# Performance work log

Measured on AMD Instinct MI355X. Metric: run time of the kernel, lower is better.

## Reference

```python
import jax, jax.numpy as jnp
import numpy as np
from jax import lax

B, C, H, W = 16, 64, 64, 64
K = 3                  # kernel_size
D_IN = C * K           # moe input dim = 192
D_OUT = 128            # out_channels
N_EXP = 8
TOP_K = 2
N_SHARED = 1


def setup_inputs() -> dict:
    key = jax.random.key(0)
    ks = jax.random.split(key, 7)
    x = jax.random.normal(ks[0], (B, C, H, W), dtype=jnp.float32)
    # depthwise conv: groups=C, each input channel -> K output channels
    conv_w = jax.random.normal(ks[1], (D_IN, 1, K, K), dtype=jnp.float32) * 0.1
    router_w = jax.random.normal(ks[2], (D_IN, N_EXP), dtype=jnp.float32) * 0.05
    w_experts = jax.random.normal(ks[3], (N_EXP, D_IN, D_OUT), dtype=jnp.float32) * 0.05
    b_experts = jnp.zeros((N_EXP, D_OUT), dtype=jnp.float32)
    w_shared = jax.random.normal(ks[4], (N_SHARED, D_IN, D_OUT), dtype=jnp.float32) * 0.05
    b_shared = jnp.zeros((N_SHARED, D_OUT), dtype=jnp.float32)
    return {"x": x, "conv_w": conv_w, "router_w": router_w,
            "w_experts": w_experts, "b_experts": b_experts,
            "w_shared": w_shared, "b_shared": b_shared}


def _moe_conv2d(x, conv_w, router_w, w_experts, b_experts, w_shared, b_shared):
    pad = K // 2
    # depthwise conv (B,C,H,W) -> (B, C*K, H, W)
    x_conv = lax.conv_general_dilated(
        x, conv_w, window_strides=(1, 1), padding=[(pad, pad), (pad, pad)],
        feature_group_count=C, dimension_numbers=("NCHW", "OIHW", "NCHW"))
    # flatten to token stream (B*H*W, D_IN)
    tokens = x_conv.transpose(0, 2, 3, 1).reshape(-1, D_IN)
    # router: softmax probs, top-k gating renormalized over selected experts
    logits = tokens @ router_w                       # (T, E)
    probs = jax.nn.softmax(logits, axis=-1)
    top_v, top_i = lax.top_k(probs, TOP_K)           # (T, k)
    gates = top_v / jnp.sum(top_v, axis=-1, keepdims=True)
    # all-expert outputs then gather the selected k per token
    expert_out = jnp.einsum("ti,eio->teo", tokens, w_experts) + b_experts  # (T, E, O)
    sel = jnp.take_along_axis(expert_out, top_i[:, :, None], axis=1)       # (T, k, O)
    y_flat = jnp.einsum("tk,tko->to", gates, sel)
    # shared experts applied to every token
    shared = jnp.einsum("ti,sio->tso", tokens, w_shared) + b_shared        # (T, S, O)
    y_flat = y_flat + jnp.sum(shared, axis=1)
    # back to feature map (B, O, H, W)
    return y_flat.reshape(B, H, W, D_OUT).transpose(0, 3, 1, 2)


def reference(x, conv_w, router_w, w_experts, b_experts, w_shared, b_shared):
    return _moe_conv2d(x, conv_w, router_w, w_experts, b_experts, w_shared, b_shared)
```

## Files before the change

kernel.cpp:

```cpp
#include <hip/hip_runtime.h>
#include <math.h>

#define BB   16
#define CC   64
#define DIN  192
#define DOUT 128
#define NEXP 8
#define NMAT 9
#define NTOK 65536
#define CAP  65568
#define SLABROWS 65552

#define TOKSTRIDE 200
#define HALFSTRIDE 104
#define LOGSTRIDE 9
#define CSTRIDE 136

typedef short bf16x8 __attribute__((ext_vector_type(8)));
typedef float f32x4  __attribute__((ext_vector_type(4)));

#define WS_TOK   0u
#define WS_WT    25165824u
#define WS_CNT   25608192u
#define WS_RT    25608256u
#define WS_RG    27706432u
#define WS_SLAB  29804608u
#define WS_TOTAL 63367232u
#define LPHALF 524288

__device__ __forceinline__ unsigned short f2bf(float f) {
    union { float f; unsigned u; } v; v.f = f;
    unsigned u = v.u;
    u += 0x7fffu + ((u >> 16) & 1u);
    return (unsigned short)(u >> 16);
}
__device__ __forceinline__ float bf2f(unsigned short s) {
    union { unsigned u; float f; } v; v.u = ((unsigned)s) << 16;
    return v.f;
}

__global__ __launch_bounds__(256)
void k1a_conv(const float* __restrict__ x,
              const float* __restrict__ conv_w,
              const float* __restrict__ router_w,
              unsigned short* __restrict__ tokbuf,
              float* __restrict__ lpart,
              int* __restrict__ cnt)
{
    __shared__ __attribute__((aligned(16))) unsigned short tokbf[64 * HALFSTRIDE];
    __shared__ float logits[64 * LOGSTRIDE];
    __shared__ __attribute__((aligned(16))) float xs[2][16 * 192];

    const int tid   = threadIdx.x;
    const int bid   = blockIdx.x;
    const int bh    = bid >> 1;
    const int chalf = bid & 1;
    const int b     = bh >> 6;
    const int h     = bh & 63;

    if (bid == 0 && tid < 16) cnt[tid] = 0;
    for (int idx = tid; idx < 64 * LOGSTRIDE; idx += 256) logits[idx] = 0.f;

    const int   h0  = (h > 0)  ? (h - 1) : 0;
    const int   h2  = (h < 63) ? (h + 1) : 63;
    const float mh0 = (h > 0)  ? 1.f : 0.f;
    const float mh2 = (h < 63) ? 1.f : 0.f;

    const int sc[3]  = { (0*256+tid)/48, (1*256+tid)/48, (2*256+tid)/48 };
    int srow[3], sseg[3];
    #pragma unroll
    for (int q = 0; q < 3; ++q) {
        int rem = (q * 256 + tid) % 48;
        srow[q] = rem >> 4; sseg[q] = rem & 15;
    }
    const float* xb = x + (size_t)b * CC * 4096;

    {
        float4 st[3];
        #pragma unroll
        for (int q = 0; q < 3; ++q) {
            int hh = (srow[q] == 0) ? h0 : ((srow[q] == 1) ? h : h2);
            st[q] = *(const float4*)(xb + ((size_t)(chalf * 32 + sc[q]) * 64 + hh) * 64
                                        + sseg[q] * 4);
        }
        #pragma unroll
        for (int q = 0; q < 3; ++q)
            *(float4*)&xs[0][sc[q] * 192 + srow[q] * 64 + sseg[q] * 4] = st[q];
    }
    __syncthreads();

    const int w  = tid & 63;
    const int cq = __builtin_amdgcn_readfirstlane(tid >> 6);

    const int   wm  = (w == 0)  ? 0  : (w - 1);
    const int   wp  = (w == 63) ? 63 : (w + 1);
    const float mwm = (w == 0)  ? 0.f : 1.f;
    const float mwp = (w == 63) ? 0.f : 1.f;

    float lacc[8];
    #pragma unroll
    for (int e = 0; e < 8; ++e) lacc[e] = 0.f;

    float4 st1[3];
    #pragma unroll
    for (int q = 0; q < 3; ++q) {
        int hh = (srow[q] == 0) ? h0 : ((srow[q] == 1) ? h : h2);
        st1[q] = *(const float4*)(xb + ((size_t)(chalf * 32 + 16 + sc[q]) * 64 + hh) * 64
                                     + sseg[q] * 4);
    }

    #pragma unroll
    for (int ch = 0; ch < 2; ++ch) {
        const float* xsc = xs[ch];
        #pragma unroll
        for (int i = 0; i < 4; ++i) {
            int cc = cq * 4 + i;
            int cl = ch * 16 + cc;
            const float* r0 = xsc + cc * 192;
            const float* r1 = r0 + 64;
            const float* r2 = r0 + 128;
            float x00 = r0[wm], x01 = r0[w], x02 = r0[wp];
            float x10 = r1[wm], x11 = r1[w], x12 = r1[wp];
            float x20 = r2[wm], x21 = r2[w], x22 = r2[wp];
            x00 *= mh0 * mwm; x01 *= mh0; x02 *= mh0 * mwp;
            x10 *= mwm;                    x12 *= mwp;
            x20 *= mh2 * mwm; x21 *= mh2; x22 *= mh2 * mwp;

            #pragma unroll
            for (int j = 0; j < 3; ++j) {
                int fl = 3 * cl + j;
                int f  = chalf * 96 + fl;
                const float* w9 = conv_w + f * 9;
                float acc = x00 * w9[0] + x01 * w9[1] + x02 * w9[2]
                          + x10 * w9[3] + x11 * w9[4] + x12 * w9[5]
                          + x20 * w9[6] + x21 * w9[7] + x22 * w9[8];
                tokbf[w * HALFSTRIDE + fl] = f2bf(acc);
                const float* rwf = router_w + f * 8;
                #pragma unroll
                for (int e = 0; e < 8; ++e) lacc[e] += acc * rwf[e];
            }
        }
        if (ch == 0) {
            #pragma unroll
            for (int q = 0; q < 3; ++q)
                *(float4*)&xs[1][sc[q] * 192 + srow[q] * 64 + sseg[q] * 4] = st1[q];
            __syncthreads();
        }
    }

    #pragma unroll
    for (int e = 0; e < 8; ++e)
        atomicAdd(&logits[w * LOGSTRIDE + e], lacc[e]);
    __syncthreads();

    for (int idx = tid; idx < 512; idx += 256) {
        int wtok = idx >> 3, e = idx & 7;
        lpart[(size_t)chalf * LPHALF + ((size_t)bh * 64 + wtok) * 8 + e] =
            logits[wtok * LOGSTRIDE + e];
    }
    for (int idx = tid; idx < 768; idx += 256) {
        int row = idx / 12, seg = idx - row * 12;
        *(bf16x8*)(tokbuf + (size_t)(bh * 64 + row) * 192 + chalf * 96 + seg * 8) =
            *(const bf16x8*)(tokbf + row * HALFSTRIDE + seg * 8);
    }
}

__global__ __launch_bounds__(256)
void k1b_route(const float* __restrict__ lpart,
               int* __restrict__ cnt,
               int* __restrict__ rowtok, float* __restrict__ rowgate,
               const float* __restrict__ w_experts,
               const float* __restrict__ w_shared,
               unsigned short* __restrict__ wt)
{
    __shared__ int lcnt[8];
    __shared__ int lbase[8];

    const int tid = threadIdx.x;
    const int blk = blockIdx.x;
    const int t   = blk * 256 + tid;

    if (tid < 8) lcnt[tid] = 0;
    __syncthreads();

    const float* p0 = lpart + (size_t)t * 8;
    const float* p1 = lpart + LPHALF + (size_t)t * 8;
    float l[8];
    #pragma unroll
    for (int e = 0; e < 8; ++e) l[e] = p0[e] + p1[e];

    int e0 = 0; float l0 = l[0];
    #pragma unroll
    for (int e = 1; e < 8; ++e) if (l[e] > l0) { l0 = l[e]; e0 = e; }
    int e1 = -1; float l1 = -INFINITY;
    #pragma unroll
    for (int e = 0; e < 8; ++e) {
        if (e == e0) continue;
        if (l[e] > l1) { l1 = l[e]; e1 = e; }
    }
    float g0 = 1.f / (1.f + expf(l1 - l0));
    float g1 = 1.f - g0;

    int r0 = atomicAdd(&lcnt[e0], 1);
    int r1 = atomicAdd(&lcnt[e1], 1);
    __syncthreads();
    if (tid < 8) lbase[tid] = atomicAdd(&cnt[tid], lcnt[tid]);
    __syncthreads();

    int p0i = e0 * CAP + lbase[e0] + r0;
    int p1i = e1 * CAP + lbase[e1] + r1;
    rowtok[p0i]  = t;
    rowgate[p0i] = g0;
    rowtok[p1i]  = t | (1 << 20);
    rowgate[p1i] = g1;

    {
        int base = blk * 864;
        for (int q = 0; q < 4; ++q) {
            int idx = base + q * 256 + tid;
            if (idx < 221184 && (q * 256 + tid) < 864) {
                int e = idx / 24576, rem = idx - e * 24576;
                int n = rem / DIN,  k  = rem - n * DIN;
                const float* src = (e < 8) ? (w_experts + (size_t)e * DIN * DOUT)
                                           : w_shared;
                wt[idx] = f2bf(src[k * DOUT + n]);
            }
        }
    }
}

__global__ __launch_bounds__(256)
void k4_routed(const unsigned short* __restrict__ tokbuf,
               const unsigned short* __restrict__ wt,
               const float* __restrict__ b_experts,
               const int* __restrict__ cnt,
               const int* __restrict__ rowtok, const float* __restrict__ rowgate,
               unsigned short* __restrict__ slab)
{
    __shared__ __attribute__((aligned(16))) unsigned short atile[2][16 * TOKSTRIDE];
    __shared__ __attribute__((aligned(16))) unsigned short ctile[2][16 * CSTRIDE];
    __shared__ int   stok[2][16];
    __shared__ float sgate[2][16];

    const int tid  = threadIdx.x;
    const int e    = blockIdx.x >> 8;
    const int jb   = blockIdx.x & 255;
    const int wave = tid >> 6;
    const int lane = tid & 63;
    const int m16  = lane & 15, quad = lane >> 4;
    const int o0   = (wave * 2 + 0) * 16 + m16;
    const int o1   = (wave * 2 + 1) * 16 + m16;

    const unsigned short* wb = wt + (size_t)e * DOUT * DIN;
    bf16x8 bfr0[6], bfr1[6];
    #pragma unroll
    for (int ks = 0; ks < 6; ++ks) {
        bfr0[ks] = *(const bf16x8*)(wb + (size_t)o0 * DIN + ks * 32 + quad * 8);
        bfr1[ks] = *(const bf16x8*)(wb + (size_t)o1 * DIN + ks * 32 + quad * 8);
    }
    const float be0 = b_experts[e * DOUT + o0];
    const float be1 = b_experts[e * DOUT + o1];

    const int cnt_e  = cnt[e];
    const int ntiles = (cnt_e + 15) >> 4;
    const int*   rt = rowtok  + e * CAP;
    const float* rg = rowgate + e * CAP;

    const int r0i = tid / 24,        s0i = tid - r0i * 24;
    const int r1i = (tid + 256) / 24, s1i = (tid + 256) - r1i * 24;
    const bool has1 = (tid + 256) < 384;

    if (jb < ntiles) {
        int base = jb * 16;
        if (tid < 16) {
            int r = base + tid;
            bool ok = (r < cnt_e);
            stok[0][tid]  = ok ? rt[r] : NTOK;
            sgate[0][tid] = ok ? rg[r] : 0.f;
        }
        {
            int ra = base + r0i;
            int raw = (ra < cnt_e) ? rt[ra] : NTOK;
            *(bf16x8*)&atile[0][r0i * TOKSTRIDE + s0i * 8] =
                *(const bf16x8*)(tokbuf + (size_t)(raw & 0x1FFFF) * 192 + s0i * 8);
            if (has1) {
                int rb = base + r1i;
                int rawb = (rb < cnt_e) ? rt[rb] : NTOK;
                *(bf16x8*)&atile[0][r1i * TOKSTRIDE + s1i * 8] =
                    *(const bf16x8*)(tokbuf + (size_t)(rawb & 0x1FFFF) * 192 + s1i * 8);
            }
        }
    }
    __syncthreads();

    int buf = 0;
    for (int j = jb; j < ntiles; j += 256, buf ^= 1) {
        const int jn = j + 256;
        const bool more = (jn < ntiles);

        bf16x8 nx0 = {0,0,0,0,0,0,0,0}, nx1 = {0,0,0,0,0,0,0,0};
        int nmt = NTOK; float nmg = 0.f;
        if (more) {
            int base = jn * 16;
            if (tid < 16) {
                int r = base + tid;
                bool ok = (r < cnt_e);
                nmt = ok ? rt[r] : NTOK;
                nmg = ok ? rg[r] : 0.f;
            }
            int ra = base + r0i;
            int rawa = (ra < cnt_e) ? rt[ra] : NTOK;
            nx0 = *(const bf16x8*)(tokbuf + (size_t)(rawa & 0x1FFFF) * 192 + s0i * 8);
            if (has1) {
                int rb = base + r1i;
                int rawb = (rb < cnt_e) ? rt[rb] : NTOK;
                nx1 = *(const bf16x8*)(tokbuf + (size_t)(rawb & 0x1FFFF) * 192 + s1i * 8);
            }
        }

        bf16x8 a[6];
        #pragma unroll
        for (int ks = 0; ks < 6; ++ks)
            a[ks] = *(const bf16x8*)&atile[buf][m16 * TOKSTRIDE + ks * 32 + quad * 8];

        f32x4 acc0 = {0.f, 0.f, 0.f, 0.f};
        f32x4 acc1 = {0.f, 0.f, 0.f, 0.f};
        #pragma unroll
        for (int ks = 0; ks < 6; ++ks) {
            acc0 = __builtin_amdgcn_mfma_f32_16x16x32_bf16(a[ks], bfr0[ks], acc0, 0, 0, 0);
            acc1 = __builtin_amdgcn_mfma_f32_16x16x32_bf16(a[ks], bfr1[ks], acc1, 0, 0, 0);
        }

        #pragma unroll
        for (int i = 0; i < 4; ++i) {
            int   row = quad * 4 + i;
            float g   = sgate[buf][row];
            ctile[buf][row * CSTRIDE + o0] = f2bf(g * (acc0[i] + be0));
            ctile[buf][row * CSTRIDE + o1] = f2bf(g * (acc1[i] + be1));
        }

        if (more) {
            if (tid < 16) { stok[buf ^ 1][tid] = nmt; sgate[buf ^ 1][tid] = nmg; }
            *(bf16x8*)&atile[buf ^ 1][r0i * TOKSTRIDE + s0i * 8] = nx0;
            if (has1) *(bf16x8*)&atile[buf ^ 1][r1i * TOKSTRIDE + s1i * 8] = nx1;
        }
        __syncthreads();

        {
            int row = tid >> 4, chk = tid & 15;
            int raw = stok[buf][row];
            int t    = raw & 0x1FFFF;
            int slot = raw >> 20;
            *(bf16x8*)(slab + (size_t)slot * SLABROWS * DOUT
                            + (size_t)t * DOUT + chk * 8) =
                *(const bf16x8*)&ctile[buf][row * CSTRIDE + chk * 8];
        }
    }
}

__global__ __launch_bounds__(256)
void k3_shared(const unsigned short* __restrict__ tokbuf,
               const unsigned short* __restrict__ wt,
               const unsigned short* __restrict__ slab,
               const float* __restrict__ b_shared,
               float* __restrict__ out)
{
    __shared__ float out_lds[32 * 129];

    const int tid  = threadIdx.x;
    const int bid  = blockIdx.x;
    const int bh   = bid >> 1;
    const int wh   = bid & 1;
    const int b    = bh >> 6;
    const int h    = bh & 63;
    const int wave = tid >> 6, lane = tid & 63;
    const int mt   = wave >> 1, nh = wave & 1;
    const int m16  = lane & 15, quad = lane >> 4;
    const int t0   = bh * 64 + wh * 32;

    bf16x8 pv0[2], pv1[2];
    {
        const unsigned short* s0 = slab;
        const unsigned short* s1 = slab + (size_t)SLABROWS * DOUT;
        #pragma unroll
        for (int it = 0; it < 2; ++it) {
            int idx = it * 256 + tid;
            int tl = idx >> 4, chk = idx & 15;
            size_t gt = (size_t)t0 + tl;
            pv0[it] = *(const bf16x8*)(s0 + gt * DOUT + chk * 8);
            pv1[it] = *(const bf16x8*)(s1 + gt * DOUT + chk * 8);
        }
    }

    const unsigned short* ap =
        tokbuf + (size_t)(t0 + mt * 16 + m16) * 192 + quad * 8;
    bf16x8 a[6];
    #pragma unroll
    for (int ks = 0; ks < 6; ++ks) a[ks] = *(const bf16x8*)(ap + ks * 32);

    const unsigned short* wsh = wt + (size_t)8 * DOUT * DIN;

    bf16x8 bcur[6], bnxt[6];
    {
        int o = (nh * 4 + 0) * 16 + m16;
        const unsigned short* bp = wsh + (size_t)o * DIN + quad * 8;
        #pragma unroll
        for (int ks = 0; ks < 6; ++ks) bcur[ks] = *(const bf16x8*)(bp + ks * 32);
    }
    #pragma unroll
    for (int nb2 = 0; nb2 < 4; ++nb2) {
        if (nb2 < 3) {
            int on = (nh * 4 + nb2 + 1) * 16 + m16;
            const unsigned short* bp = wsh + (size_t)on * DIN + quad * 8;
            #pragma unroll
            for (int ks = 0; ks < 6; ++ks) bnxt[ks] = *(const bf16x8*)(bp + ks * 32);
        }
        int o = (nh * 4 + nb2) * 16 + m16;
        f32x4 acc = {0.f, 0.f, 0.f, 0.f};
        #pragma unroll
        for (int ks = 0; ks < 6; ++ks)
            acc = __builtin_amdgcn_mfma_f32_16x16x32_bf16(a[ks], bcur[ks], acc, 0, 0, 0);
        float bs = b_shared[o];
        #pragma unroll
        for (int i = 0; i < 4; ++i) {
            int tloc = mt * 16 + quad * 4 + i;
            out_lds[tloc * 129 + o] = acc[i] + bs;
        }
        #pragma unroll
        for (int ks = 0; ks < 6; ++ks) bcur[ks] = bnxt[ks];
    }
    __syncthreads();

    #pragma unroll
    for (int it = 0; it < 2; ++it) {
        int idx = it * 256 + tid;
        int tl = idx >> 4, chk = idx & 15;
        float* dst = &out_lds[tl * 129 + chk * 8];
        #pragma unroll
        for (int q = 0; q < 8; ++q)
            dst[q] += bf2f((unsigned short)pv0[it][q])
                    + bf2f((unsigned short)pv1[it][q]);
    }
    __syncthreads();

    float* outp = out + ((size_t)b * DOUT) * 4096 + h * 64 + wh * 32;
    for (int idx = tid; idx < 32 * DOUT; idx += 256) {
        int wloc = idx & 31, o = idx >> 5;
        outp[(size_t)o * 4096 + wloc] = out_lds[wloc * 129 + o];
    }
}

#define OUTSTRIDE 129
#define MAXROWS 320
#define MAXTILES 20

__global__ __launch_bounds__(256)
void moe_conv2d_mfma(const float* __restrict__ x,
                     const float* __restrict__ conv_w,
                     const float* __restrict__ router_w,
                     const unsigned short* __restrict__ wt,
                     const float* __restrict__ b_experts,
                     const float* __restrict__ b_shared,
                     float* __restrict__ out)
{
    __shared__ __attribute__((aligned(16))) unsigned short tokbf[64 * TOKSTRIDE];
    __shared__ float out_lds[64 * OUTSTRIDE];
    __shared__ float rw[DIN * NEXP];
    __shared__ float logits[64 * LOGSTRIDE];
    __shared__ float sg0[64], sg1[64];
    __shared__ int   se0[64], se1[64];
    __shared__ int   rowtok[MAXROWS];
    __shared__ float rowgate[MAXROWS];
    __shared__ int   cbuf[NMAT];
    __shared__ int   tilexp[MAXTILES], tilebase[MAXTILES];
    __shared__ int   ntiles_s;

    const int tid = threadIdx.x;
    const int bh  = blockIdx.x;
    const int b   = bh >> 6;
    const int h   = bh & 63;

    for (int idx = tid; idx < DIN * NEXP; idx += 256) rw[idx] = router_w[idx];
    for (int idx = tid; idx < 64 * LOGSTRIDE; idx += 256) logits[idx] = 0.f;
    __syncthreads();
    {
        const int w  = tid & 63;
        const int fq = tid >> 6;
        float lacc[8];
        #pragma unroll
        for (int e = 0; e < 8; ++e) lacc[e] = 0.f;
        for (int i = 0; i < 48; ++i) {
            int f = i * 4 + fq;
            int c = f / 3;
            const float* wp    = conv_w + f * 9;
            const float* xbase = x + ((size_t)(b * 64 + c) * 64) * 64;
            float acc = 0.f;
            #pragma unroll
            for (int kh = 0; kh < 3; ++kh) {
                int hh = h + kh - 1;
                if (hh < 0 || hh > 63) continue;
                const float* xrow = xbase + hh * 64;
                #pragma unroll
                for (int kw = 0; kw < 3; ++kw) {
                    int ww = w + kw - 1;
                    if (ww < 0 || ww > 63) continue;
                    acc += xrow[ww] * wp[kh * 3 + kw];
                }
            }
            tokbf[w * TOKSTRIDE + f] = f2bf(acc);
            const float* rwf = rw + f * 8;
            #pragma unroll
            for (int e = 0; e < 8; ++e) lacc[e] += acc * rwf[e];
        }
        #pragma unroll
        for (int e = 0; e < 8; ++e)
            atomicAdd(&logits[w * LOGSTRIDE + e], lacc[e]);
    }
    __syncthreads();
    if (tid < 64) {
        int w = tid;
        float l[8];
        #pragma unroll
        for (int e = 0; e < 8; ++e) l[e] = logits[w * LOGSTRIDE + e];
        int e0 = 0; float l0 = l[0];
        #pragma unroll
        for (int e = 1; e < 8; ++e) if (l[e] > l0) { l0 = l[e]; e0 = e; }
        int e1 = -1; float l1 = -INFINITY;
        #pragma unroll
        for (int e = 0; e < 8; ++e) {
            if (e == e0) continue;
            if (l[e] > l1) { l1 = l[e]; e1 = e; }
        }
        float g0 = 1.f / (1.f + expf(l1 - l0));
        sg0[w] = g0; sg1[w] = 1.f - g0;
        se0[w] = e0; se1[w] = e1;
    }
    __syncthreads();
    for (int idx = tid; idx < 64 * DOUT; idx += 256) {
        int t = idx >> 7, o = idx & 127;
        out_lds[t * OUTSTRIDE + o] = b_shared[o]
            + sg0[t] * b_experts[se0[t] * DOUT + o]
            + sg1[t] * b_experts[se1[t] * DOUT + o];
    }
    if (tid < 8) {
        int c = 0;
        for (int t = 0; t < 64; ++t) c += (se0[t] == tid) + (se1[t] == tid);
        cbuf[tid] = c;
    } else if (tid == 8) cbuf[8] = 64;
    __syncthreads();
    if (tid < NMAT) {
        int e = tid;
        int start = 0, tb = 0;
        for (int e2 = 0; e2 < e; ++e2) {
            int ce = cbuf[e2];
            int tl = (ce + 15) >> 4;
            start += tl << 4; tb += tl;
        }
        int ce = cbuf[e];
        int tl = (ce + 15) >> 4;
        for (int j = 0; j < tl; ++j) { tilexp[tb + j] = e; tilebase[tb + j] = start + (j << 4); }
        if (e == 8) ntiles_s = tb + tl;
        int j = 0;
        if (e < 8) {
            for (int t = 0; t < 64; ++t) {
                if (se0[t] == e) { rowtok[start + j] = t; rowgate[start + j] = sg0[t]; ++j; }
                if (se1[t] == e) { rowtok[start + j] = t; rowgate[start + j] = sg1[t]; ++j; }
            }
        } else {
            for (int t = 0; t < 64; ++t) { rowtok[start + j] = t; rowgate[start + j] = 1.f; ++j; }
        }
        for (; j < (tl << 4); ++j) { rowtok[start + j] = 0; rowgate[start + j] = 0.f; }
    }
    __syncthreads();
    {
        const int wave = tid >> 6;
        const int lane = tid & 63;
        const int m16  = lane & 15;
        const int quad = lane >> 4;
        const int nt   = ntiles_s;
        for (int ti = wave; ti < nt; ti += 4) {
            int e    = tilexp[ti];
            int base = tilebase[ti];
            int tA = rowtok[base + m16];
            bf16x8 a[6];
            #pragma unroll
            for (int ks = 0; ks < 6; ++ks)
                a[ks] = *(const bf16x8*)(tokbf + tA * TOKSTRIDE + ks * 32 + quad * 8);
            int st[4]; float sgt[4];
            #pragma unroll
            for (int i2 = 0; i2 < 4; ++i2) {
                int r = base + quad * 4 + i2;
                st[i2] = rowtok[r]; sgt[i2] = rowgate[r];
            }
            const unsigned short* we = wt + (size_t)e * DOUT * DIN;
            for (int n = 0; n < 8; ++n) {
                const unsigned short* wp = we + (size_t)(n * 16 + m16) * DIN + quad * 8;
                f32x4 acc = {0.f, 0.f, 0.f, 0.f};
                #pragma unroll
                for (int ks = 0; ks < 6; ++ks) {
                    bf16x8 bfr2 = *(const bf16x8*)(wp + ks * 32);
                    acc = __builtin_amdgcn_mfma_f32_16x16x32_bf16(a[ks], bfr2, acc, 0, 0, 0);
                }
                int ncol = n * 16 + m16;
                #pragma unroll
                for (int i2 = 0; i2 < 4; ++i2)
                    atomicAdd(&out_lds[st[i2] * OUTSTRIDE + ncol], sgt[i2] * acc[i2]);
            }
        }
    }
    __syncthreads();
    {
        float* outp = out + (((size_t)b * DOUT) * 64 + h) * 64;
        for (int idx = tid; idx < 64 * DOUT; idx += 256) {
            int w = idx & 63, o = idx >> 6;
            outp[(size_t)o * 4096 + w] = out_lds[w * OUTSTRIDE + o];
        }
    }
}

__global__ __launch_bounds__(256)
void prep_weights_only(const float* __restrict__ w_experts,
                       const float* __restrict__ w_shared,
                       unsigned short* __restrict__ wt)
{
    int e = blockIdx.x;
    const float* src = (e < 8) ? (w_experts + (size_t)e * DIN * DOUT) : w_shared;
    unsigned short* dst = wt + (size_t)e * DOUT * DIN;
    for (int idx = threadIdx.x; idx < DOUT * DIN; idx += 256) {
        int n = idx / DIN, k = idx - n * DIN;
        dst[idx] = f2bf(src[k * DOUT + n]);
    }
}

extern "C" void kernel_launch(void* const* d_in, const int* in_sizes, int n_in,
                              void* d_out, int out_size, void* d_ws, size_t ws_size,
                              hipStream_t stream)
{
    const float* x         = (const float*)d_in[0];
    const float* conv_w    = (const float*)d_in[1];
    const float* router_w  = (const float*)d_in[2];
    const float* w_experts = (const float*)d_in[3];
    const float* b_experts = (const float*)d_in[4];
    const float* w_shared  = (const float*)d_in[5];
    const float* b_shared  = (const float*)d_in[6];
    float* out = (float*)d_out;
    char* ws = (char*)d_ws;

    if (ws_size >= WS_TOTAL) {
        unsigned short* tokbuf  = (unsigned short*)(ws + WS_TOK);
        unsigned short* wt      = (unsigned short*)(ws + WS_WT);
        int*            cnt     = (int*)(ws + WS_CNT);
        int*            rowtok  = (int*)(ws + WS_RT);
        float*          rowgate = (float*)(ws + WS_RG);
        unsigned short* slab    = (unsigned short*)(ws + WS_SLAB);
        float*          lpart   = (float*)(ws + WS_SLAB);

        k1a_conv<<<dim3(2048), dim3(256), 0, stream>>>(
            x, conv_w, router_w, tokbuf, lpart, cnt);
        k1b_route<<<dim3(256), dim3(256), 0, stream>>>(
            lpart, cnt, rowtok, rowgate, w_experts, w_shared, wt);
        k4_routed<<<dim3(2048), dim3(256), 0, stream>>>(
            tokbuf, wt, b_experts, cnt, rowtok, rowgate, slab);
        k3_shared<<<dim3(2048), dim3(256), 0, stream>>>(
            tokbuf, wt, slab, b_shared, out);
    } else {
        unsigned short* wt = (unsigned short*)ws;
        prep_weights_only<<<dim3(NMAT), dim3(256), 0, stream>>>(w_experts, w_shared, wt);
        moe_conv2d_mfma<<<dim3(1024), dim3(256), 0, stream>>>(
            x, conv_w, router_w, wt, b_experts, b_shared, out);
    }
}
```

Measured before the change: 179.3 us.

## Fuse conv with routing and fold shared expert into routed GEMM kernel

The conv and routing kernels are merged, so each block computes its 32 tokens' full 192-dim features and logits, does top-2 selection and expert-slot assignment in place, and no longer writes and re-reads partial logits. The counter reset moves to a memset. When the workspace is large enough, the shared expert runs as a ninth dense 'expert' inside the routed MFMA kernel, writing to a third slab. A light combine kernel then sums the three slabs and transposes to NCHW. This trades the heavier shared-GEMM epilogue for extra slab traffic, and it needs a larger workspace or else falls back to the old path.

```diff
diff --git a/kernel.cpp b/kernel.cpp
--- a/kernel.cpp
+++ b/kernel.cpp
@@ -12,7 +12,6 @@
 #define SLABROWS 65552
 
 #define TOKSTRIDE 200
-#define HALFSTRIDE 104
 #define LOGSTRIDE 9
 #define CSTRIDE 136
 
@@ -25,8 +24,8 @@
 #define WS_RT    25608256u
 #define WS_RG    27706432u
 #define WS_SLAB  29804608u
-#define WS_TOTAL 63367232u
-#define LPHALF 524288
+#define WS_TOTAL  63367232u
+#define WS_TOTAL3 80148544u
 
 __device__ __forceinline__ unsigned short f2bf(float f) {
     union { float f; unsigned u; } v; v.f = f;
@@ -40,202 +39,173 @@
 }
 
 __global__ __launch_bounds__(256)
-void k1a_conv(const float* __restrict__ x,
-              const float* __restrict__ conv_w,
-              const float* __restrict__ router_w,
-              unsigned short* __restrict__ tokbuf,
-              float* __restrict__ lpart,
-              int* __restrict__ cnt)
-{
-    __shared__ __attribute__((aligned(16))) unsigned short tokbf[64 * HALFSTRIDE];
-    __shared__ float logits[64 * LOGSTRIDE];
-    __shared__ __attribute__((aligned(16))) float xs[2][16 * 192];
-
-    const int tid   = threadIdx.x;
-    const int bid   = blockIdx.x;
-    const int bh    = bid >> 1;
-    const int chalf = bid & 1;
-    const int b     = bh >> 6;
-    const int h     = bh & 63;
-
-    if (bid == 0 && tid < 16) cnt[tid] = 0;
-    for (int idx = tid; idx < 64 * LOGSTRIDE; idx += 256) logits[idx] = 0.f;
-
-    const int   h0  = (h > 0)  ? (h - 1) : 0;
-    const int   h2  = (h < 63) ? (h + 1) : 63;
-    const float mh0 = (h > 0)  ? 1.f : 0.f;
-    const float mh2 = (h < 63) ? 1.f : 0.f;
-
-    const int sc[3]  = { (0*256+tid)/48, (1*256+tid)/48, (2*256+tid)/48 };
-    int srow[3], sseg[3];
-    #pragma unroll
-    for (int q = 0; q < 3; ++q) {
-        int rem = (q * 256 + tid) % 48;
-        srow[q] = rem >> 4; sseg[q] = rem & 15;
-    }
-    const float* xb = x + (size_t)b * CC * 4096;
-
-    {
-        float4 st[3];
-        #pragma unroll
-        for (int q = 0; q < 3; ++q) {
-            int hh = (srow[q] == 0) ? h0 : ((srow[q] == 1) ? h : h2);
-            st[q] = *(const float4*)(xb + ((size_t)(chalf * 32 + sc[q]) * 64 + hh) * 64
-                                        + sseg[q] * 4);
-        }
-        #pragma unroll
-        for (int q = 0; q < 3; ++q)
-            *(float4*)&xs[0][sc[q] * 192 + srow[q] * 64 + sseg[q] * 4] = st[q];
-    }
-    __syncthreads();
-
-    const int w  = tid & 63;
-    const int cq = __builtin_amdgcn_readfirstlane(tid >> 6);
-
-    const int   wm  = (w == 0)  ? 0  : (w - 1);
-    const int   wp  = (w == 63) ? 63 : (w + 1);
-    const float mwm = (w == 0)  ? 0.f : 1.f;
-    const float mwp = (w == 63) ? 0.f : 1.f;
-
-    float lacc[8];
-    #pragma unroll
-    for (int e = 0; e < 8; ++e) lacc[e] = 0.f;
-
-    float4 st1[3];
-    #pragma unroll
-    for (int q = 0; q < 3; ++q) {
-        int hh = (srow[q] == 0) ? h0 : ((srow[q] == 1) ? h : h2);
-        st1[q] = *(const float4*)(xb + ((size_t)(chalf * 32 + 16 + sc[q]) * 64 + hh) * 64
-                                     + sseg[q] * 4);
-    }
-
-    #pragma unroll
-    for (int ch = 0; ch < 2; ++ch) {
-        const float* xsc = xs[ch];
-        #pragma unroll
-        for (int i = 0; i < 4; ++i) {
-            int cc = cq * 4 + i;
-            int cl = ch * 16 + cc;
-            const float* r0 = xsc + cc * 192;
-            const float* r1 = r0 + 64;
-            const float* r2 = r0 + 128;
-            float x00 = r0[wm], x01 = r0[w], x02 = r0[wp];
-            float x10 = r1[wm], x11 = r1[w], x12 = r1[wp];
-            float x20 = r2[wm], x21 = r2[w], x22 = r2[wp];
-            x00 *= mh0 * mwm; x01 *= mh0; x02 *= mh0 * mwp;
-            x10 *= mwm;                    x12 *= mwp;
-            x20 *= mh2 * mwm; x21 *= mh2; x22 *= mh2 * mwp;
-
-            #pragma unroll
-            for (int j = 0; j < 3; ++j) {
-                int fl = 3 * cl + j;
-                int f  = chalf * 96 + fl;
-                const float* w9 = conv_w + f * 9;
-                float acc = x00 * w9[0] + x01 * w9[1] + x02 * w9[2]
-                          + x10 * w9[3] + x11 * w9[4] + x12 * w9[5]
-                          + x20 * w9[6] + x21 * w9[7] + x22 * w9[8];
-                tokbf[w * HALFSTRIDE + fl] = f2bf(acc);
-                const float* rwf = router_w + f * 8;
-                #pragma unroll
-                for (int e = 0; e < 8; ++e) lacc[e] += acc * rwf[e];
-            }
-        }
-        if (ch == 0) {
-            #pragma unroll
-            for (int q = 0; q < 3; ++q)
-                *(float4*)&xs[1][sc[q] * 192 + srow[q] * 64 + sseg[q] * 4] = st1[q];
-            __syncthreads();
-        }
-    }
-
-    #pragma unroll
-    for (int e = 0; e < 8; ++e)
-        atomicAdd(&logits[w * LOGSTRIDE + e], lacc[e]);
-    __syncthreads();
-
-    for (int idx = tid; idx < 512; idx += 256) {
-        int wtok = idx >> 3, e = idx & 7;
-        lpart[(size_t)chalf * LPHALF + ((size_t)bh * 64 + wtok) * 8 + e] =
-            logits[wtok * LOGSTRIDE + e];
-    }
-    for (int idx = tid; idx < 768; idx += 256) {
-        int row = idx / 12, seg = idx - row * 12;
-        *(bf16x8*)(tokbuf + (size_t)(bh * 64 + row) * 192 + chalf * 96 + seg * 8) =
-            *(const bf16x8*)(tokbf + row * HALFSTRIDE + seg * 8);
-    }
-}
-
-__global__ __launch_bounds__(256)
-void k1b_route(const float* __restrict__ lpart,
+void k1a_fused(const float* __restrict__ x,
+               const float* __restrict__ conv_w,
+               const float* __restrict__ router_w,
+               unsigned short* __restrict__ tokbuf,
                int* __restrict__ cnt,
                int* __restrict__ rowtok, float* __restrict__ rowgate,
                const float* __restrict__ w_experts,
                const float* __restrict__ w_shared,
                unsigned short* __restrict__ wt)
 {
-    __shared__ int lcnt[8];
-    __shared__ int lbase[8];
-
-    const int tid = threadIdx.x;
-    const int blk = blockIdx.x;
-    const int t   = blk * 256 + tid;
+    __shared__ __attribute__((aligned(16))) float xs[2][1920];
+    __shared__ __attribute__((aligned(16))) unsigned short tokbf[32 * TOKSTRIDE];
+    __shared__ float logits[32 * LOGSTRIDE];
+    __shared__ int lcnt[8], lbase[8];
+
+    const int tid   = threadIdx.x;
+    const int bid   = blockIdx.x;
+    const int bh    = bid >> 1;
+    const int wh    = bid & 1;
+    const int b     = bh >> 6;
+    const int h     = bh & 63;
+    const int wbase = wh * 32;
+    const int t0    = bh * 64 + wbase;
 
     if (tid < 8) lcnt[tid] = 0;
-    __syncthreads();
-
-    const float* p0 = lpart + (size_t)t * 8;
-    const float* p1 = lpart + LPHALF + (size_t)t * 8;
-    float l[8];
-    #pragma unroll
-    for (int e = 0; e < 8; ++e) l[e] = p0[e] + p1[e];
-
-    int e0 = 0; float l0 = l[0];
-    #pragma unroll
-    for (int e = 1; e < 8; ++e) if (l[e] > l0) { l0 = l[e]; e0 = e; }
-    int e1 = -1; float l1 = -INFINITY;
-    #pragma unroll
-    for (int e = 0; e < 8; ++e) {
-        if (e == e0) continue;
-        if (l[e] > l1) { l1 = l[e]; e1 = e; }
-    }
-    float g0 = 1.f / (1.f + expf(l1 - l0));
-    float g1 = 1.f - g0;
-
-    int r0 = atomicAdd(&lcnt[e0], 1);
-    int r1 = atomicAdd(&lcnt[e1], 1);
+    for (int idx = tid; idx < 32 * LOGSTRIDE; idx += 256) logits[idx] = 0.f;
+
+    const int   h0  = (h > 0)  ? (h - 1) : 0;
+    const int   h2  = (h < 63) ? (h + 1) : 63;
+    const float mh0 = (h > 0)  ? 1.f : 0.f;
+    const float mh2 = (h < 63) ? 1.f : 0.f;
+
+    const float* xb = x + (size_t)b * CC * 4096;
+
+    int sc[2], sr[2], ss[2], sc4[2]; bool sv[2];
+    #pragma unroll
+    for (int q = 0; q < 2; ++q) {
+        int idx = q * 256 + tid;
+        sv[q] = idx < 480;
+        int c16 = idx / 30, rem = idx % 30;
+        sc[q] = c16; sr[q] = rem / 10; ss[q] = rem % 10;
+        int c4 = (wbase >> 2) + ss[q] - 1;
+        sc4[q] = c4 < 0 ? 0 : (c4 > 15 ? 15 : c4);
+    }
+
+    #pragma unroll
+    for (int q = 0; q < 2; ++q) if (sv[q]) {
+        int hh = (sr[q] == 0) ? h0 : ((sr[q] == 1) ? h : h2);
+        float4 v = *(const float4*)(xb + ((size_t)sc[q] * 64 + hh) * 64 + sc4[q] * 4);
+        *(float4*)&xs[0][sc[q] * 120 + sr[q] * 40 + ss[q] * 4] = v;
+    }
+    __syncthreads();
+
+    const int wloc = tid & 31;
+    const int cg   = tid >> 5;
+    const int w    = wbase + wloc;
+    const float mwm = (w == 0)  ? 0.f : 1.f;
+    const float mwp = (w == 63) ? 0.f : 1.f;
+
+    float lacc[8];
+    #pragma unroll
+    for (int e = 0; e < 8; ++e) lacc[e] = 0.f;
+
+    int buf = 0;
+    for (int ck = 0; ck < 4; ++ck) {
+        float4 st[2];
+        if (ck < 3) {
+            #pragma unroll
+            for (int q = 0; q < 2; ++q) if (sv[q]) {
+                int hh = (sr[q] == 0) ? h0 : ((sr[q] == 1) ? h : h2);
+                st[q] = *(const float4*)(xb + ((size_t)((ck + 1) * 16 + sc[q]) * 64 + hh) * 64
+                                            + sc4[q] * 4);
+            }
+        }
+        #pragma unroll
+        for (int i = 0; i < 2; ++i) {
+            int cc = cg * 2 + i;
+            int c  = ck * 16 + cc;
+            const float* r0 = &xs[buf][cc * 120];
+            const float* r1 = r0 + 40;
+            const float* r2 = r0 + 80;
+            float x00 = r0[wloc+3], x01 = r0[wloc+4], x02 = r0[wloc+5];
+            float x10 = r1[wloc+3], x11 = r1[wloc+4], x12 = r1[wloc+5];
+            float x20 = r2[wloc+3], x21 = r2[wloc+4], x22 = r2[wloc+5];
+            x00 *= mh0 * mwm; x01 *= mh0; x02 *= mh0 * mwp;
+            x10 *= mwm;                    x12 *= mwp;
+            x20 *= mh2 * mwm; x21 *= mh2; x22 *= mh2 * mwp;
+            #pragma unroll
+            for (int j = 0; j < 3; ++j) {
+                int f = 3 * c + j;
+                const float* w9 = conv_w + f * 9;
+                float acc = x00 * w9[0] + x01 * w9[1] + x02 * w9[2]
+                          + x10 * w9[3] + x11 * w9[4] + x12 * w9[5]
+                          + x20 * w9[6] + x21 * w9[7] + x22 * w9[8];
+                tokbf[wloc * TOKSTRIDE + f] = f2bf(acc);
+                const float* rwf = router_w + f * 8;
+                #pragma unroll
+                for (int e = 0; e < 8; ++e) lacc[e] += acc * rwf[e];
+            }
+        }
+        if (ck < 3) {
+            #pragma unroll
+            for (int q = 0; q < 2; ++q) if (sv[q])
+                *(float4*)&xs[buf ^ 1][sc[q] * 120 + sr[q] * 40 + ss[q] * 4] = st[q];
+            __syncthreads();
+            buf ^= 1;
+        }
+    }
+    #pragma unroll
+    for (int e = 0; e < 8; ++e)
+        atomicAdd(&logits[wloc * LOGSTRIDE + e], lacc[e]);
+    __syncthreads();
+
+    int e0r = 0, e1r = 0, r0r = 0, r1r = 0; float g0r = 0.f, g1r = 0.f;
+    if (tid < 32) {
+        float l[8];
+        #pragma unroll
+        for (int e = 0; e < 8; ++e) l[e] = logits[tid * LOGSTRIDE + e];
+        int e0 = 0; float l0 = l[0];
+        #pragma unroll
+        for (int e = 1; e < 8; ++e) if (l[e] > l0) { l0 = l[e]; e0 = e; }
+        int e1 = -1; float l1 = -INFINITY;
+        #pragma unroll
+        for (int e = 0; e < 8; ++e) {
+            if (e == e0) continue;
+            if (l[e] > l1) { l1 = l[e]; e1 = e; }
+        }
+        float g0 = 1.f / (1.f + expf(l1 - l0));
+        e0r = e0; e1r = e1; g0r = g0; g1r = 1.f - g0;
+        r0r = atomicAdd(&lcnt[e0], 1);
+        r1r = atomicAdd(&lcnt[e1], 1);
+    }
     __syncthreads();
     if (tid < 8) lbase[tid] = atomicAdd(&cnt[tid], lcnt[tid]);
     __syncthreads();
-
-    int p0i = e0 * CAP + lbase[e0] + r0;
-    int p1i = e1 * CAP + lbase[e1] + r1;
-    rowtok[p0i]  = t;
-    rowgate[p0i] = g0;
-    rowtok[p1i]  = t | (1 << 20);
-    rowgate[p1i] = g1;
-
-    {
-        int base = blk * 864;
-        for (int q = 0; q < 4; ++q) {
-            int idx = base + q * 256 + tid;
-            if (idx < 221184 && (q * 256 + tid) < 864) {
-                int e = idx / 24576, rem = idx - e * 24576;
-                int n = rem / DIN,  k  = rem - n * DIN;
-                const float* src = (e < 8) ? (w_experts + (size_t)e * DIN * DOUT)
-                                           : w_shared;
-                wt[idx] = f2bf(src[k * DOUT + n]);
-            }
-        }
+    if (tid < 32) {
+        int t = t0 + tid;
+        int i0 = e0r * CAP + lbase[e0r] + r0r;
+        rowtok[i0] = t;              rowgate[i0] = g0r;
+        int i1 = e1r * CAP + lbase[e1r] + r1r;
+        rowtok[i1] = t | (1 << 20);  rowgate[i1] = g1r;
+    }
+
+    #pragma unroll
+    for (int q = 0; q < 3; ++q) {
+        int idx = q * 256 + tid;
+        int row = idx / 24, seg = idx - row * 24;
+        *(bf16x8*)(tokbuf + (size_t)(t0 + row) * 192 + seg * 8) =
+            *(const bf16x8*)(tokbf + row * TOKSTRIDE + seg * 8);
+    }
+    if (tid < 108) {
+        int idx = bid * 108 + tid;
+        int e = idx / 24576, rem = idx - e * 24576;
+        int n = rem / DIN, k = rem - n * DIN;
+        const float* src = (e < 8) ? (w_experts + (size_t)e * DIN * DOUT) : w_shared;
+        wt[idx] = f2bf(src[k * DOUT + n]);
     }
 }
 
 __global__ __launch_bounds__(256)
-void k4_routed(const unsigned short* __restrict__ tokbuf,
-               const unsigned short* __restrict__ wt,
-               const float* __restrict__ b_experts,
-               const int* __restrict__ cnt,
-               const int* __restrict__ rowtok, const float* __restrict__ rowgate,
-               unsigned short* __restrict__ slab)
+void k4_all(const unsigned short* __restrict__ tokbuf,
+            const unsigned short* __restrict__ wt,
+            const float* __restrict__ b_experts,
+            const float* __restrict__ b_shared,
+            const int* __restrict__ cnt,
+            const int* __restrict__ rowtok, const float* __restrict__ rowgate,
+            unsigned short* __restrict__ slab)
 {
     __shared__ __attribute__((aligned(16))) unsigned short atile[2][16 * TOKSTRIDE];
     __shared__ __attribute__((aligned(16))) unsigned short ctile[2][16 * CSTRIDE];
@@ -243,8 +213,11 @@
     __shared__ float sgate[2][16];
 
     const int tid  = threadIdx.x;
-    const int e    = blockIdx.x >> 8;
-    const int jb   = blockIdx.x & 255;
+    int e, jb, jstep;
+    if (blockIdx.x < 2048) { e = blockIdx.x >> 8; jb = blockIdx.x & 255; jstep = 256; }
+    else                   { e = 8; jb = blockIdx.x - 2048; jstep = 1024; }
+    const bool dense = (e == 8);
+
     const int wave = tid >> 6;
     const int lane = tid & 63;
     const int m16  = lane & 15, quad = lane >> 4;
@@ -258,34 +231,33 @@
         bfr0[ks] = *(const bf16x8*)(wb + (size_t)o0 * DIN + ks * 32 + quad * 8);
         bfr1[ks] = *(const bf16x8*)(wb + (size_t)o1 * DIN + ks * 32 + quad * 8);
     }
-    const float be0 = b_experts[e * DOUT + o0];
-    const float be1 = b_experts[e * DOUT + o1];
-
-    const int cnt_e  = cnt[e];
+    const float be0 = dense ? b_shared[o0] : b_experts[e * DOUT + o0];
+    const float be1 = dense ? b_shared[o1] : b_experts[e * DOUT + o1];
+
+    const int cnt_e  = dense ? NTOK : cnt[e];
     const int ntiles = (cnt_e + 15) >> 4;
     const int*   rt = rowtok  + e * CAP;
     const float* rg = rowgate + e * CAP;
 
-    const int r0i = tid / 24,        s0i = tid - r0i * 24;
+    const int r0i = tid / 24,         s0i = tid - r0i * 24;
     const int r1i = (tid + 256) / 24, s1i = (tid + 256) - r1i * 24;
     const bool has1 = (tid + 256) < 384;
+
+    #define FETCH_RAW(r) (dense ? ((r) | (2 << 20)) : (((r) < cnt_e) ? rt[r] : NTOK))
+    #define FETCH_G(r)   (dense ? 1.f : (((r) < cnt_e) ? rg[r] : 0.f))
 
     if (jb < ntiles) {
         int base = jb * 16;
         if (tid < 16) {
-            int r = base + tid;
-            bool ok = (r < cnt_e);
-            stok[0][tid]  = ok ? rt[r] : NTOK;
-            sgate[0][tid] = ok ? rg[r] : 0.f;
+            stok[0][tid]  = FETCH_RAW(base + tid);
+            sgate[0][tid] = FETCH_G(base + tid);
         }
         {
-            int ra = base + r0i;
-            int raw = (ra < cnt_e) ? rt[ra] : NTOK;
+            int rawa = FETCH_RAW(base + r0i);
             *(bf16x8*)&atile[0][r0i * TOKSTRIDE + s0i * 8] =
-                *(const bf16x8*)(tokbuf + (size_t)(raw & 0x1FFFF) * 192 + s0i * 8);
+                *(const bf16x8*)(tokbuf + (size_t)(rawa & 0x1FFFF) * 192 + s0i * 8);
             if (has1) {
-                int rb = base + r1i;
-                int rawb = (rb < cnt_e) ? rt[rb] : NTOK;
+                int rawb = FETCH_RAW(base + r1i);
                 *(bf16x8*)&atile[0][r1i * TOKSTRIDE + s1i * 8] =
                     *(const bf16x8*)(tokbuf + (size_t)(rawb & 0x1FFFF) * 192 + s1i * 8);
             }
@@ -294,26 +266,19 @@
     __syncthreads();
 
     int buf = 0;
-    for (int j = jb; j < ntiles; j += 256, buf ^= 1) {
-        const int jn = j + 256;
+    for (int j = jb; j < ntiles; j += jstep, buf ^= 1) {
+        const int jn = j + jstep;
         const bool more = (jn < ntiles);
 
         bf16x8 nx0 = {0,0,0,0,0,0,0,0}, nx1 = {0,0,0,0,0,0,0,0};
         int nmt = NTOK; float nmg = 0.f;
         if (more) {
             int base = jn * 16;
-            if (tid < 16) {
-                int r = base + tid;
-                bool ok = (r < cnt_e);
-                nmt = ok ? rt[r] : NTOK;
-                nmg = ok ? rg[r] : 0.f;
-            }
-            int ra = base + r0i;
-            int rawa = (ra < cnt_e) ? rt[ra] : NTOK;
+            if (tid < 16) { nmt = FETCH_RAW(base + tid); nmg = FETCH_G(base + tid); }
+            int rawa = FETCH_RAW(base + r0i);
             nx0 = *(const bf16x8*)(tokbuf + (size_t)(rawa & 0x1FFFF) * 192 + s0i * 8);
             if (has1) {
-                int rb = base + r1i;
-                int rawb = (rb < cnt_e) ? rt[rb] : NTOK;
+                int rawb = FETCH_RAW(base + r1i);
                 nx1 = *(const bf16x8*)(tokbuf + (size_t)(rawb & 0x1FFFF) * 192 + s1i * 8);
             }
         }
@@ -355,6 +320,49 @@
                             + (size_t)t * DOUT + chk * 8) =
                 *(const bf16x8*)&ctile[buf][row * CSTRIDE + chk * 8];
         }
+    }
+    #undef FETCH_RAW
+    #undef FETCH_G
+}
+
+__global__ __launch_bounds__(256)
+void k3_combine(const unsigned short* __restrict__ slab,
+                float* __restrict__ out)
+{
+    __shared__ float out_lds[32 * 129];
+
+    const int tid = threadIdx.x;
+    const int bid = blockIdx.x;
+    const int bh  = bid >> 1;
+    const int wh  = bid & 1;
+    const int b   = bh >> 6;
+    const int h   = bh & 63;
+    const int t0  = bh * 64 + wh * 32;
+
+    const unsigned short* s0 = slab;
+    const unsigned short* s1 = slab + (size_t)SLABROWS * DOUT;
+    const unsigned short* s2 = slab + (size_t)2 * SLABROWS * DOUT;
+
+    #pragma unroll
+    for (int it = 0; it < 2; ++it) {
+        int idx = it * 256 + tid;
+        int tl = idx >> 4, chk = idx & 15;
+        size_t gt = (size_t)t0 + tl;
+        bf16x8 v0 = *(const bf16x8*)(s0 + gt * DOUT + chk * 8);
+        bf16x8 v1 = *(const bf16x8*)(s1 + gt * DOUT + chk * 8);
+        bf16x8 v2 = *(const bf16x8*)(s2 + gt * DOUT + chk * 8);
+        float* dst = &out_lds[tl * 129 + chk * 8];
+        #pragma unroll
+        for (int q = 0; q < 8; ++q)
+            dst[q] = bf2f((unsigned short)v0[q]) + bf2f((unsigned short)v1[q])
+                   + bf2f((unsigned short)v2[q]);
+    }
+    __syncthreads();
+
+    float* outp = out + ((size_t)b * DOUT) * 4096 + h * 64 + wh * 32;
+    for (int idx = tid; idx < 32 * DOUT; idx += 256) {
+        int wloc = idx & 31, o = idx >> 5;
+        outp[(size_t)o * 4096 + wloc] = out_lds[wloc * 129 + o];
     }
 }
 
@@ -653,16 +661,21 @@
         int*            rowtok  = (int*)(ws + WS_RT);
         float*          rowgate = (float*)(ws + WS_RG);
         unsigned short* slab    = (unsigned short*)(ws + WS_SLAB);
-        float*          lpart   = (float*)(ws + WS_SLAB);
-
-        k1a_conv<<<dim3(2048), dim3(256), 0, stream>>>(
-            x, conv_w, router_w, tokbuf, lpart, cnt);
-        k1b_route<<<dim3(256), dim3(256), 0, stream>>>(
-            lpart, cnt, rowtok, rowgate, w_experts, w_shared, wt);
-        k4_routed<<<dim3(2048), dim3(256), 0, stream>>>(
-            tokbuf, wt, b_experts, cnt, rowtok, rowgate, slab);
-        k3_shared<<<dim3(2048), dim3(256), 0, stream>>>(
-            tokbuf, wt, slab, b_shared, out);
+
+        hipMemsetAsync(cnt, 0, 64, stream);
+        k1a_fused<<<dim3(2048), dim3(256), 0, stream>>>(
+            x, conv_w, router_w, tokbuf, cnt, rowtok, rowgate,
+            w_experts, w_shared, wt);
+        if (ws_size >= WS_TOTAL3) {
+            k4_all<<<dim3(3072), dim3(256), 0, stream>>>(
+                tokbuf, wt, b_experts, b_shared, cnt, rowtok, rowgate, slab);
+            k3_combine<<<dim3(2048), dim3(256), 0, stream>>>(slab, out);
+        } else {
+            k4_all<<<dim3(2048), dim3(256), 0, stream>>>(
+                tokbuf, wt, b_experts, b_shared, cnt, rowtok, rowgate, slab);
+            k3_shared<<<dim3(2048), dim3(256), 0, stream>>>(
+                tokbuf, wt, slab, b_shared, out);
+        }
     } else {
         unsigned short* wt = (unsigned short*)ws;
         prep_weights_only<<<dim3(NMAT), dim3(256), 0, stream>>>(w_experts, w_shared, wt);
```

Result: slower. 199.6 us (+11.3%).

## Fold shared-expert GEMM into routed kernel, add lightweight combine kernel

Applied to the files above, without the earlier changes.

The shared-expert matmul moves into the routed MFMA kernel as 1024 extra dense blocks (expert index 8) that write a third bf16 slab. A new, simple combine kernel then sums the three slabs and transposes into NCHW output. This lets shared and routed GEMM work share one launch and balance across the GPU, and keeps the final kernel as pure memory traffic. It costs a larger workspace (an extra slab write and read), rounds the shared output to bf16, and only runs when the workspace is big enough.

```diff
diff --git a/kernel.cpp b/kernel.cpp
--- a/kernel.cpp
+++ b/kernel.cpp
@@ -25,7 +25,8 @@
 #define WS_RT    25608256u
 #define WS_RG    27706432u
 #define WS_SLAB  29804608u
-#define WS_TOTAL 63367232u
+#define WS_TOTAL  63367232u
+#define WS_TOTAL3 80148544u
 #define LPHALF 524288
 
 __device__ __forceinline__ unsigned short f2bf(float f) {
@@ -230,12 +231,13 @@
 }
 
 __global__ __launch_bounds__(256)
-void k4_routed(const unsigned short* __restrict__ tokbuf,
-               const unsigned short* __restrict__ wt,
-               const float* __restrict__ b_experts,
-               const int* __restrict__ cnt,
-               const int* __restrict__ rowtok, const float* __restrict__ rowgate,
-               unsigned short* __restrict__ slab)
+void k4_all(const unsigned short* __restrict__ tokbuf,
+            const unsigned short* __restrict__ wt,
+            const float* __restrict__ b_experts,
+            const float* __restrict__ b_shared,
+            const int* __restrict__ cnt,
+            const int* __restrict__ rowtok, const float* __restrict__ rowgate,
+            unsigned short* __restrict__ slab)
 {
     __shared__ __attribute__((aligned(16))) unsigned short atile[2][16 * TOKSTRIDE];
     __shared__ __attribute__((aligned(16))) unsigned short ctile[2][16 * CSTRIDE];
@@ -243,8 +245,11 @@
     __shared__ float sgate[2][16];
 
     const int tid  = threadIdx.x;
-    const int e    = blockIdx.x >> 8;
-    const int jb   = blockIdx.x & 255;
+    int e, jb, jstep;
+    if (blockIdx.x < 2048) { e = blockIdx.x >> 8; jb = blockIdx.x & 255; jstep = 256; }
+    else                   { e = 8; jb = blockIdx.x - 2048; jstep = 1024; }
+    const bool dense = (e == 8);
+
     const int wave = tid >> 6;
     const int lane = tid & 63;
     const int m16  = lane & 15, quad = lane >> 4;
@@ -258,34 +263,33 @@
         bfr0[ks] = *(const bf16x8*)(wb + (size_t)o0 * DIN + ks * 32 + quad * 8);
         bfr1[ks] = *(const bf16x8*)(wb + (size_t)o1 * DIN + ks * 32 + quad * 8);
     }
-    const float be0 = b_experts[e * DOUT + o0];
-    const float be1 = b_experts[e * DOUT + o1];
-
-    const int cnt_e  = cnt[e];
+    const float be0 = dense ? b_shared[o0] : b_experts[e * DOUT + o0];
+    const float be1 = dense ? b_shared[o1] : b_experts[e * DOUT + o1];
+
+    const int cnt_e  = dense ? NTOK : cnt[e];
     const int ntiles = (cnt_e + 15) >> 4;
     const int*   rt = rowtok  + e * CAP;
     const float* rg = rowgate + e * CAP;
 
-    const int r0i = tid / 24,        s0i = tid - r0i * 24;
+    const int r0i = tid / 24,         s0i = tid - r0i * 24;
     const int r1i = (tid + 256) / 24, s1i = (tid + 256) - r1i * 24;
     const bool has1 = (tid + 256) < 384;
+
+    #define FETCH_RAW(r) (dense ? ((r) | (2 << 20)) : (((r) < cnt_e) ? rt[r] : NTOK))
+    #define FETCH_G(r)   (dense ? 1.f : (((r) < cnt_e) ? rg[r] : 0.f))
 
     if (jb < ntiles) {
         int base = jb * 16;
         if (tid < 16) {
-            int r = base + tid;
-            bool ok = (r < cnt_e);
-            stok[0][tid]  = ok ? rt[r] : NTOK;
-            sgate[0][tid] = ok ? rg[r] : 0.f;
+            stok[0][tid]  = FETCH_RAW(base + tid);
+            sgate[0][tid] = FETCH_G(base + tid);
         }
         {
-            int ra = base + r0i;
-            int raw = (ra < cnt_e) ? rt[ra] : NTOK;
+            int rawa = FETCH_RAW(base + r0i);
             *(bf16x8*)&atile[0][r0i * TOKSTRIDE + s0i * 8] =
-                *(const bf16x8*)(tokbuf + (size_t)(raw & 0x1FFFF) * 192 + s0i * 8);
+                *(const bf16x8*)(tokbuf + (size_t)(rawa & 0x1FFFF) * 192 + s0i * 8);
             if (has1) {
-                int rb = base + r1i;
-                int rawb = (rb < cnt_e) ? rt[rb] : NTOK;
+                int rawb = FETCH_RAW(base + r1i);
                 *(bf16x8*)&atile[0][r1i * TOKSTRIDE + s1i * 8] =
                     *(const bf16x8*)(tokbuf + (size_t)(rawb & 0x1FFFF) * 192 + s1i * 8);
             }
@@ -294,26 +298,19 @@
     __syncthreads();
 
     int buf = 0;
-    for (int j = jb; j < ntiles; j += 256, buf ^= 1) {
-        const int jn = j + 256;
+    for (int j = jb; j < ntiles; j += jstep, buf ^= 1) {
+        const int jn = j + jstep;
         const bool more = (jn < ntiles);
 
         bf16x8 nx0 = {0,0,0,0,0,0,0,0}, nx1 = {0,0,0,0,0,0,0,0};
         int nmt = NTOK; float nmg = 0.f;
         if (more) {
             int base = jn * 16;
-            if (tid < 16) {
-                int r = base + tid;
-                bool ok = (r < cnt_e);
-                nmt = ok ? rt[r] : NTOK;
-                nmg = ok ? rg[r] : 0.f;
-            }
-            int ra = base + r0i;
-            int rawa = (ra < cnt_e) ? rt[ra] : NTOK;
+            if (tid < 16) { nmt = FETCH_RAW(base + tid); nmg = FETCH_G(base + tid); }
+            int rawa = FETCH_RAW(base + r0i);
             nx0 = *(const bf16x8*)(tokbuf + (size_t)(rawa & 0x1FFFF) * 192 + s0i * 8);
             if (has1) {
-                int rb = base + r1i;
-                int rawb = (rb < cnt_e) ? rt[rb] : NTOK;
+                int rawb = FETCH_RAW(base + r1i);
                 nx1 = *(const bf16x8*)(tokbuf + (size_t)(rawb & 0x1FFFF) * 192 + s1i * 8);
             }
         }
@@ -355,6 +352,49 @@
                             + (size_t)t * DOUT + chk * 8) =
                 *(const bf16x8*)&ctile[buf][row * CSTRIDE + chk * 8];
         }
+    }
+    #undef FETCH_RAW
+    #undef FETCH_G
+}
+
+__global__ __launch_bounds__(256)
+void k3_combine(const unsigned short* __restrict__ slab,
+                float* __restrict__ out)
+{
+    __shared__ float out_lds[32 * 129];
+
+    const int tid = threadIdx.x;
+    const int bid = blockIdx.x;
+    const int bh  = bid >> 1;
+    const int wh  = bid & 1;
+    const int b   = bh >> 6;
+    const int h   = bh & 63;
+    const int t0  = bh * 64 + wh * 32;
+
+    const unsigned short* s0 = slab;
+    const unsigned short* s1 = slab + (size_t)SLABROWS * DOUT;
+    const unsigned short* s2 = slab + (size_t)2 * SLABROWS * DOUT;
+
+    #pragma unroll
+    for (int it = 0; it < 2; ++it) {
+        int idx = it * 256 + tid;
+        int tl = idx >> 4, chk = idx & 15;
+        size_t gt = (size_t)t0 + tl;
+        bf16x8 v0 = *(const bf16x8*)(s0 + gt * DOUT + chk * 8);
+        bf16x8 v1 = *(const bf16x8*)(s1 + gt * DOUT + chk * 8);
+        bf16x8 v2 = *(const bf16x8*)(s2 + gt * DOUT + chk * 8);
+        float* dst = &out_lds[tl * 129 + chk * 8];
+        #pragma unroll
+        for (int q = 0; q < 8; ++q)
+            dst[q] = bf2f((unsigned short)v0[q]) + bf2f((unsigned short)v1[q])
+                   + bf2f((unsigned short)v2[q]);
+    }
+    __syncthreads();
+
+    float* outp = out + ((size_t)b * DOUT) * 4096 + h * 64 + wh * 32;
+    for (int idx = tid; idx < 32 * DOUT; idx += 256) {
+        int wloc = idx & 31, o = idx >> 5;
+        outp[(size_t)o * 4096 + wloc] = out_lds[wloc * 129 + o];
     }
 }
 
@@ -659,10 +699,16 @@
             x, conv_w, router_w, tokbuf, lpart, cnt);
         k1b_route<<<dim3(256), dim3(256), 0, stream>>>(
             lpart, cnt, rowtok, rowgate, w_experts, w_shared, wt);
-        k4_routed<<<dim3(2048), dim3(256), 0, stream>>>(
-            tokbuf, wt, b_experts, cnt, rowtok, rowgate, slab);
-        k3_shared<<<dim3(2048), dim3(256), 0, stream>>>(
-            tokbuf, wt, slab, b_shared, out);
+        if (ws_size >= WS_TOTAL3) {
+            k4_all<<<dim3(3072), dim3(256), 0, stream>>>(
+                tokbuf, wt, b_experts, b_shared, cnt, rowtok, rowgate, slab);
+            k3_combine<<<dim3(2048), dim3(256), 0, stream>>>(slab, out);
+        } else {
+            k4_all<<<dim3(2048), dim3(256), 0, stream>>>(
+                tokbuf, wt, b_experts, b_shared, cnt, rowtok, rowgate, slab);
+            k3_shared<<<dim3(2048), dim3(256), 0, stream>>>(
+                tokbuf, wt, slab, b_shared, out);
+        }
     } else {
         unsigned short* wt = (unsigned short*)ws;
         prep_weights_only<<<dim3(NMAT), dim3(256), 0, stream>>>(w_experts, w_shared, wt);
```

Result: faster. 168.6 us (-6.0%).
